# Kernel tuning notes

Measured on AMD Instinct MI355X. Metric: run time of the kernel, lower is better.

## Reference

```python
import jax, jax.numpy as jnp
import numpy as np

NR_EMB = 1024
B_COMMITMENT = 1.0


def setup_inputs() -> dict:
    key = jax.random.key(0)
    k1, k2 = jax.random.split(key)
    inpt = jax.random.normal(k1, (64, 2048, 64), dtype=jnp.float32)
    # VarianceScaling(uniform) over shape (D, K): limit = sqrt(3*scale/fan_in), scale=1, fan_in=D
    D = 64
    limit = np.sqrt(3.0 / D).astype(np.float32)
    emb_mtrx = jax.random.uniform(k2, (D, NR_EMB), dtype=jnp.float32, minval=-limit, maxval=limit)
    return {"inpt": inpt, "emb_mtrx": emb_mtrx}


def reference(inpt, emb_mtrx):
    D = inpt.shape[-1]
    x = inpt.reshape(-1, D)  # [N, D]
    dist = (jnp.sum(x * x, axis=1, keepdims=True)
            - 2.0 * (x @ emb_mtrx)
            + jnp.sum(emb_mtrx * emb_mtrx, axis=0, keepdims=True))
    idx = jnp.argmax(-dist, axis=1)  # [N]
    # avg_probs = mean of one-hot over N == normalized histogram (same math, no N x K one-hot)
    avg_probs = jnp.bincount(idx, length=NR_EMB).astype(inpt.dtype) / x.shape[0]
    perplexity = jnp.exp(-jnp.sum(avg_probs * jnp.log(avg_probs + 1e-10)))
    idx_nd = idx.reshape(inpt.shape[:-1])  # [B, T]
    q = jnp.take(emb_mtrx.T, idx_nd, axis=0)  # gather codebook rows -> [B, T, D]
    l_commitment = jnp.mean((jax.lax.stop_gradient(q) - inpt) ** 2)
    l_codebook = jnp.mean((q - jax.lax.stop_gradient(inpt)) ** 2)
    loss = B_COMMITMENT * l_commitment + l_codebook
    q = inpt + jax.lax.stop_gradient(q - inpt)  # straight-through estimator
    return q, loss, perplexity
```

## Files before the change

kernel.cpp:

```cpp
#include <hip/hip_runtime.h>

#define NROWS 131072
#define D 64
#define K 1024

typedef __attribute__((ext_vector_type(8))) short short8;
typedef __attribute__((ext_vector_type(4))) float f32x4;
typedef unsigned int u32;


__device__ __forceinline__ unsigned short f2bf_rne(float f) {
    u32 u = __float_as_uint(f);
    u += 0x7fff + ((u >> 16) & 1);
    return (unsigned short)(u >> 16);
}

__device__ __forceinline__ float b2f(short s) {
    return __uint_as_float(((u32)(unsigned short)s) << 16);
}

__global__ __launch_bounds__(256) void prep_kernel(const float* __restrict__ E,
                                                   unsigned short* __restrict__ ehT,
                                                   float* __restrict__ e2g,
                                                   int* __restrict__ hist) {
    __shared__ float ps[4][64];
    const int lane = threadIdx.x & 63;
    const int w = threadIdx.x >> 6;
    const int k = blockIdx.x * 64 + lane;
    float s = 0.f;
#pragma unroll
    for (int half = 0; half < 2; ++half) {
        short8 h8;
#pragma unroll
        for (int j = 0; j < 8; ++j) {
            float v = E[(w * 16 + half * 8 + j) * K + k];
            s = fmaf(v, v, s);
            h8[j] = (short)f2bf_rne(v);
        }
        *(short8*)(ehT + (size_t)k * D + w * 16 + half * 8) = h8;
    }
    ps[w][lane] = s;
    __syncthreads();
    if (w == 0) e2g[k] = -0.5f * (ps[0][lane] + ps[1][lane] + ps[2][lane] + ps[3][lane]);
    if (threadIdx.x < 64) hist[blockIdx.x * 64 + threadIdx.x] = 0;
}

__global__ __launch_bounds__(1024) void score_kernel(const float* __restrict__ X,
                                                     const unsigned short* __restrict__ ehT,
                                                     const float* __restrict__ e2g,
                                                     int* __restrict__ hist,
                                                     float* __restrict__ wavesum,
                                                     float* __restrict__ q) {
    __shared__ unsigned short xbuf[2][8192];
    __shared__ float mrg[2][128 * 17];
    __shared__ int idxl[2][128];
    __shared__ float redL[16];

    const int tid = threadIdx.x;
    const int wave = tid >> 6;
    const int lane = tid & 63;
    const int quad = lane >> 4;
    const int lc = lane & 15;
    const size_t row0 = (size_t)blockIdx.x * 512;

    const int st = tid >> 7, so = (tid >> 4) & 7, sl = tid & 15;
    const int rowl = st * 16 + sl;
    const float* sbase = X + (row0 + (size_t)rowl) * D + so * 8;

    {
        float4 La = *(const float4*)(sbase);
        float4 Lb = *(const float4*)(sbase + 4);
        union { u32 u[4]; short8 v; } pk;
        pk.u[0] = __builtin_amdgcn_perm(__float_as_uint(La.y), __float_as_uint(La.x), 0x07060302);
        pk.u[1] = __builtin_amdgcn_perm(__float_as_uint(La.w), __float_as_uint(La.z), 0x07060302);
        pk.u[2] = __builtin_amdgcn_perm(__float_as_uint(Lb.y), __float_as_uint(Lb.x), 0x07060302);
        pk.u[3] = __builtin_amdgcn_perm(__float_as_uint(Lb.w), __float_as_uint(Lb.z), 0x07060302);
        *(short8*)((char*)&xbuf[0][0] + tid * 16) = pk.v;
    }

    const int cbase = wave * 64;
    short8 ae[4][2];
    f32x4 e2f[4];
#pragma unroll
    for (int ct = 0; ct < 4; ++ct) {
        const unsigned short* ap = ehT + ((size_t)(cbase + ct * 16 + lc) << 6) + quad * 8;
        ae[ct][0] = *(const short8*)(ap);
        ae[ct][1] = *(const short8*)(ap + 32);
        e2f[ct] = *(const f32x4*)(e2g + cbase + ct * 16 + quad * 4);
    }
    const u32 cb0 = (u32)(cbase + quad * 4);

    __syncthreads();

    float ls = 0.f;
    for (int c = 0; c < 4; ++c) {
        const int cur = c & 1;
        float4 La, Lb;
        if (c < 3) {
            La = *(const float4*)(sbase + (c + 1) * 8192);
            Lb = *(const float4*)(sbase + (c + 1) * 8192 + 4);
        }

        float bt8[8];
        const char* bb = (const char*)&xbuf[cur][0];
#pragma unroll 2
        for (int t = 0; t < 8; ++t) {
            const char* bp = bb + t * 2048 + quad * 256 + lc * 16;
            short8 b0 = *(const short8*)(bp);
            short8 b1 = *(const short8*)(bp + 1024);
            float bt = -3.4e38f;
#pragma unroll
            for (int ct = 0; ct < 4; ++ct) {
                f32x4 acc = __builtin_amdgcn_mfma_f32_16x16x32_bf16(ae[ct][0], b0, e2f[ct], 0, 0, 0);
                acc = __builtin_amdgcn_mfma_f32_16x16x32_bf16(ae[ct][1], b1, acc, 0, 0, 0);
                float p0 = __uint_as_float((__float_as_uint(acc[0]) & 0xFFFFFC00u) | (cb0 + ct * 16 + 0));
                float p1 = __uint_as_float((__float_as_uint(acc[1]) & 0xFFFFFC00u) | (cb0 + ct * 16 + 1));
                float p2 = __uint_as_float((__float_as_uint(acc[2]) & 0xFFFFFC00u) | (cb0 + ct * 16 + 2));
                float p3 = __uint_as_float((__float_as_uint(acc[3]) & 0xFFFFFC00u) | (cb0 + ct * 16 + 3));
                bt = fmaxf(bt, fmaxf(p0, p1));
                bt = fmaxf(bt, fmaxf(p2, p3));
            }
            bt8[t] = bt;
        }
#pragma unroll
        for (int t = 0; t < 8; ++t) {
            float bt = bt8[t];
            bt = fmaxf(bt, __shfl_xor(bt, 16, 64));
            bt = fmaxf(bt, __shfl_xor(bt, 32, 64));
            if (lane < 16) mrg[cur][(t * 16 + lane) * 17 + wave] = bt;
        }
        __syncthreads();

        if (tid < 128) {
            float m = mrg[cur][tid * 17];
#pragma unroll
            for (int w = 1; w < 16; ++w) m = fmaxf(m, mrg[cur][tid * 17 + w]);
            int kk = (int)(__float_as_uint(m) & 1023u);
            idxl[cur][tid] = kk;
            atomicAdd(&hist[kk], 1);
        }
        if (c < 3) {
            union { u32 u[4]; short8 v; } pk;
            pk.u[0] = __builtin_amdgcn_perm(__float_as_uint(La.y), __float_as_uint(La.x), 0x07060302);
            pk.u[1] = __builtin_amdgcn_perm(__float_as_uint(La.w), __float_as_uint(La.z), 0x07060302);
            pk.u[2] = __builtin_amdgcn_perm(__float_as_uint(Lb.y), __float_as_uint(Lb.x), 0x07060302);
            pk.u[3] = __builtin_amdgcn_perm(__float_as_uint(Lb.w), __float_as_uint(Lb.z), 0x07060302);
            *(short8*)((char*)&xbuf[cur ^ 1][0] + tid * 16) = pk.v;
        }
        __syncthreads();

        {
            int kk = idxl[cur][rowl];
            short8 ev = *(const short8*)(ehT + ((size_t)kk << 6) + so * 8);
            short8 xv = *(const short8*)(&xbuf[cur][tid * 8]);
            float4 qa, qb;
            float e0, dd;
            e0 = b2f(ev[0]); dd = e0 - b2f(xv[0]); ls = fmaf(dd, dd, ls); qa.x = e0;
            e0 = b2f(ev[1]); dd = e0 - b2f(xv[1]); ls = fmaf(dd, dd, ls); qa.y = e0;
            e0 = b2f(ev[2]); dd = e0 - b2f(xv[2]); ls = fmaf(dd, dd, ls); qa.z = e0;
            e0 = b2f(ev[3]); dd = e0 - b2f(xv[3]); ls = fmaf(dd, dd, ls); qa.w = e0;
            e0 = b2f(ev[4]); dd = e0 - b2f(xv[4]); ls = fmaf(dd, dd, ls); qb.x = e0;
            e0 = b2f(ev[5]); dd = e0 - b2f(xv[5]); ls = fmaf(dd, dd, ls); qb.y = e0;
            e0 = b2f(ev[6]); dd = e0 - b2f(xv[6]); ls = fmaf(dd, dd, ls); qb.z = e0;
            e0 = b2f(ev[7]); dd = e0 - b2f(xv[7]); ls = fmaf(dd, dd, ls); qb.w = e0;
            float* qp = q + (row0 + (size_t)(c * 128 + rowl)) * D + so * 8;
            *(float4*)(qp) = qa;
            *(float4*)(qp + 4) = qb;
        }
    }

    for (int off = 32; off > 0; off >>= 1) ls += __shfl_down(ls, off, 64);
    if (lane == 0) redL[wave] = ls;
    __syncthreads();
    if (tid == 0) {
        float L = 0.f;
#pragma unroll
        for (int i = 0; i < 16; ++i) L += redL[i];
        wavesum[blockIdx.x] = L;
    }
}

__global__ __launch_bounds__(1024) void finalize_kernel(const int* __restrict__ hist,
                                                        const float* __restrict__ wavesum,
                                                        float* __restrict__ out) {
    __shared__ float redH[16], redL[16];
    int tid = threadIdx.x;
    float p = (float)hist[tid] * (1.0f / (float)NROWS);
    float term = p * logf(p + 1e-10f);
    float ls = (tid < 256) ? wavesum[tid] : 0.f;
    for (int off = 32; off > 0; off >>= 1) {
        term += __shfl_down(term, off, 64);
        ls += __shfl_down(ls, off, 64);
    }
    int lane = tid & 63, wid = tid >> 6;
    if (lane == 0) { redH[wid] = term; redL[wid] = ls; }
    __syncthreads();
    if (tid == 0) {
        float H = 0.f, L = 0.f;
#pragma unroll
        for (int i = 0; i < 16; ++i) { H += redH[i]; L += redL[i]; }
        out[(size_t)NROWS * D + 0] = 2.0f * (L / (float)(NROWS * D));
        out[(size_t)NROWS * D + 1] = expf(-H);
    }
}

extern "C" void kernel_launch(void* const* d_in, const int* in_sizes, int n_in,
                              void* d_out, int out_size, void* d_ws, size_t ws_size,
                              hipStream_t stream) {
    const float* X = (const float*)d_in[0];
    const float* E = (const float*)d_in[1];
    float* out = (float*)d_out;

    char* w = (char*)d_ws;
    unsigned short* ehT = (unsigned short*)(w + 0);
    float* e2g          = (float*)(w + 131072);
    int* hist           = (int*)(w + 135168);
    float* wavesum      = (float*)(w + 139264);

    prep_kernel<<<16, 256, 0, stream>>>(E, ehT, e2g, hist);
    score_kernel<<<NROWS / 512, 1024, 0, stream>>>(X, ehT, e2g, hist, wavesum, out);
    finalize_kernel<<<1, 1024, 0, stream>>>(hist, wavesum, out);
}
```

Measured before the change: 123.9 us.

## Process rows in two 256-row superchunks to halve block barriers

The score loop now handles two 128-row chunks per iteration (256 rows), so there are two super-iterations instead of four. This halves the number of __syncthreads and merge phases. X staging is quadruple-buffered: two chunks are preloaded up front and the other two are loaded during the first super-iteration. The shuffle-reduce of the per-tile max is moved into the MFMA loop, and the histogram atomics are moved after the barrier. In exchange, LDS use grows (64KB of xbuf plus a larger mrg), which can lower occupancy, and the prefetch is less deeply overlapped since chunks 2 and 3 are both loaded at the start.

```diff
diff --git a/kernel.cpp b/kernel.cpp
--- a/kernel.cpp
+++ b/kernel.cpp
@@ -51,9 +51,9 @@
                                                      int* __restrict__ hist,
                                                      float* __restrict__ wavesum,
                                                      float* __restrict__ q) {
-    __shared__ unsigned short xbuf[2][8192];
-    __shared__ float mrg[2][128 * 17];
-    __shared__ int idxl[2][128];
+    __shared__ unsigned short xbuf[4][8192];
+    __shared__ float mrg[256 * 17];
+    __shared__ int idxl[2][256];
     __shared__ float redL[16];
 
     const int tid = threadIdx.x;
@@ -68,14 +68,21 @@
     const float* sbase = X + (row0 + (size_t)rowl) * D + so * 8;
 
     {
-        float4 La = *(const float4*)(sbase);
-        float4 Lb = *(const float4*)(sbase + 4);
+        float4 L0a = *(const float4*)(sbase);
+        float4 L0b = *(const float4*)(sbase + 4);
+        float4 L1a = *(const float4*)(sbase + 8192);
+        float4 L1b = *(const float4*)(sbase + 8192 + 4);
         union { u32 u[4]; short8 v; } pk;
-        pk.u[0] = __builtin_amdgcn_perm(__float_as_uint(La.y), __float_as_uint(La.x), 0x07060302);
-        pk.u[1] = __builtin_amdgcn_perm(__float_as_uint(La.w), __float_as_uint(La.z), 0x07060302);
-        pk.u[2] = __builtin_amdgcn_perm(__float_as_uint(Lb.y), __float_as_uint(Lb.x), 0x07060302);
-        pk.u[3] = __builtin_amdgcn_perm(__float_as_uint(Lb.w), __float_as_uint(Lb.z), 0x07060302);
+        pk.u[0] = __builtin_amdgcn_perm(__float_as_uint(L0a.y), __float_as_uint(L0a.x), 0x07060302);
+        pk.u[1] = __builtin_amdgcn_perm(__float_as_uint(L0a.w), __float_as_uint(L0a.z), 0x07060302);
+        pk.u[2] = __builtin_amdgcn_perm(__float_as_uint(L0b.y), __float_as_uint(L0b.x), 0x07060302);
+        pk.u[3] = __builtin_amdgcn_perm(__float_as_uint(L0b.w), __float_as_uint(L0b.z), 0x07060302);
         *(short8*)((char*)&xbuf[0][0] + tid * 16) = pk.v;
+        pk.u[0] = __builtin_amdgcn_perm(__float_as_uint(L1a.y), __float_as_uint(L1a.x), 0x07060302);
+        pk.u[1] = __builtin_amdgcn_perm(__float_as_uint(L1a.w), __float_as_uint(L1a.z), 0x07060302);
+        pk.u[2] = __builtin_amdgcn_perm(__float_as_uint(L1b.y), __float_as_uint(L1b.x), 0x07060302);
+        pk.u[3] = __builtin_amdgcn_perm(__float_as_uint(L1b.w), __float_as_uint(L1b.z), 0x07060302);
+        *(short8*)((char*)&xbuf[1][0] + tid * 16) = pk.v;
     }
 
     const int cbase = wave * 64;
@@ -93,18 +100,18 @@
     __syncthreads();
 
     float ls = 0.f;
-    for (int c = 0; c < 4; ++c) {
-        const int cur = c & 1;
-        float4 La, Lb;
-        if (c < 3) {
-            La = *(const float4*)(sbase + (c + 1) * 8192);
-            Lb = *(const float4*)(sbase + (c + 1) * 8192 + 4);
-        }
-
-        float bt8[8];
-        const char* bb = (const char*)&xbuf[cur][0];
+    float4 P2a, P2b, P3a, P3b;
+    for (int sc = 0; sc < 2; ++sc) {
+        if (sc == 0) {
+            P2a = *(const float4*)(sbase + 2 * 8192);
+            P2b = *(const float4*)(sbase + 2 * 8192 + 4);
+            P3a = *(const float4*)(sbase + 3 * 8192);
+            P3b = *(const float4*)(sbase + 3 * 8192 + 4);
+        }
+
+        const char* bb = (const char*)&xbuf[sc * 2][0];
 #pragma unroll 2
-        for (int t = 0; t < 8; ++t) {
+        for (int t = 0; t < 16; ++t) {
             const char* bp = bb + t * 2048 + quad * 256 + lc * 16;
             short8 b0 = *(const short8*)(bp);
             short8 b1 = *(const short8*)(bp + 1024);
@@ -120,39 +127,41 @@
                 bt = fmaxf(bt, fmaxf(p0, p1));
                 bt = fmaxf(bt, fmaxf(p2, p3));
             }
-            bt8[t] = bt;
-        }
-#pragma unroll
-        for (int t = 0; t < 8; ++t) {
-            float bt = bt8[t];
             bt = fmaxf(bt, __shfl_xor(bt, 16, 64));
             bt = fmaxf(bt, __shfl_xor(bt, 32, 64));
-            if (lane < 16) mrg[cur][(t * 16 + lane) * 17 + wave] = bt;
+            if (lane < 16) mrg[(t * 16 + lane) * 17 + wave] = bt;
         }
         __syncthreads();
 
-        if (tid < 128) {
-            float m = mrg[cur][tid * 17];
-#pragma unroll
-            for (int w = 1; w < 16; ++w) m = fmaxf(m, mrg[cur][tid * 17 + w]);
-            int kk = (int)(__float_as_uint(m) & 1023u);
-            idxl[cur][tid] = kk;
-            atomicAdd(&hist[kk], 1);
-        }
-        if (c < 3) {
+        if (tid < 256) {
+            float m = mrg[tid * 17];
+#pragma unroll
+            for (int w = 1; w < 16; ++w) m = fmaxf(m, mrg[tid * 17 + w]);
+            idxl[sc][tid] = (int)(__float_as_uint(m) & 1023u);
+        }
+        if (sc == 0) {
             union { u32 u[4]; short8 v; } pk;
-            pk.u[0] = __builtin_amdgcn_perm(__float_as_uint(La.y), __float_as_uint(La.x), 0x07060302);
-            pk.u[1] = __builtin_amdgcn_perm(__float_as_uint(La.w), __float_as_uint(La.z), 0x07060302);
-            pk.u[2] = __builtin_amdgcn_perm(__float_as_uint(Lb.y), __float_as_uint(Lb.x), 0x07060302);
-            pk.u[3] = __builtin_amdgcn_perm(__float_as_uint(Lb.w), __float_as_uint(Lb.z), 0x07060302);
-            *(short8*)((char*)&xbuf[cur ^ 1][0] + tid * 16) = pk.v;
+            pk.u[0] = __builtin_amdgcn_perm(__float_as_uint(P2a.y), __float_as_uint(P2a.x), 0x07060302);
+            pk.u[1] = __builtin_amdgcn_perm(__float_as_uint(P2a.w), __float_as_uint(P2a.z), 0x07060302);
+            pk.u[2] = __builtin_amdgcn_perm(__float_as_uint(P2b.y), __float_as_uint(P2b.x), 0x07060302);
+            pk.u[3] = __builtin_amdgcn_perm(__float_as_uint(P2b.w), __float_as_uint(P2b.z), 0x07060302);
+            *(short8*)((char*)&xbuf[2][0] + tid * 16) = pk.v;
+            pk.u[0] = __builtin_amdgcn_perm(__float_as_uint(P3a.y), __float_as_uint(P3a.x), 0x07060302);
+            pk.u[1] = __builtin_amdgcn_perm(__float_as_uint(P3a.w), __float_as_uint(P3a.z), 0x07060302);
+            pk.u[2] = __builtin_amdgcn_perm(__float_as_uint(P3b.y), __float_as_uint(P3b.x), 0x07060302);
+            pk.u[3] = __builtin_amdgcn_perm(__float_as_uint(P3b.w), __float_as_uint(P3b.z), 0x07060302);
+            *(short8*)((char*)&xbuf[3][0] + tid * 16) = pk.v;
         }
         __syncthreads();
 
-        {
-            int kk = idxl[cur][rowl];
+        if (tid < 256) atomicAdd(&hist[idxl[sc][tid]], 1);
+
+#pragma unroll
+        for (int h = 0; h < 2; ++h) {
+            const int cc = sc * 2 + h;
+            int kk = idxl[sc][h * 128 + rowl];
             short8 ev = *(const short8*)(ehT + ((size_t)kk << 6) + so * 8);
-            short8 xv = *(const short8*)(&xbuf[cur][tid * 8]);
+            short8 xv = *(const short8*)(&xbuf[cc][tid * 8]);
             float4 qa, qb;
             float e0, dd;
             e0 = b2f(ev[0]); dd = e0 - b2f(xv[0]); ls = fmaf(dd, dd, ls); qa.x = e0;
@@ -163,7 +172,7 @@
             e0 = b2f(ev[5]); dd = e0 - b2f(xv[5]); ls = fmaf(dd, dd, ls); qb.y = e0;
             e0 = b2f(ev[6]); dd = e0 - b2f(xv[6]); ls = fmaf(dd, dd, ls); qb.z = e0;
             e0 = b2f(ev[7]); dd = e0 - b2f(xv[7]); ls = fmaf(dd, dd, ls); qb.w = e0;
-            float* qp = q + (row0 + (size_t)(c * 128 + rowl)) * D + so * 8;
+            float* qp = q + (row0 + (size_t)(cc * 128 + rowl)) * D + so * 8;
             *(float4*)(qp) = qa;
             *(float4*)(qp + 4) = qb;
         }
```

After: 127.5 us. 1.03x slower.

## Fuse codebook prep into score kernel and use per-block shared histograms

Applied to the files above, without the earlier changes.

Removes the separate prep kernel: each score block now reads the fp32 codebook directly, converts it to bf16 in registers and computes the codebook norms with wave shuffles. Global histogram atomics are replaced by shared-memory atomics, with each block writing its own histogram, which the finalize kernel sums across 256 blocks. The gather for q reads fp32 codebook columns with a strided access pattern instead of the packed bf16 rows. This saves one launch and the global atomic contention, but adds redundant codebook conversion in every block, uncoalesced strided gathers, and a 1 MB per-block histogram reduction done by a single finalize block.

```diff
diff --git a/kernel.cpp b/kernel.cpp
--- a/kernel.cpp
+++ b/kernel.cpp
@@ -3,6 +3,7 @@
 #define NROWS 131072
 #define D 64
 #define K 1024
+#define NBLK 256
 
 typedef __attribute__((ext_vector_type(8))) short short8;
 typedef __attribute__((ext_vector_type(4))) float f32x4;
@@ -19,41 +20,15 @@
     return __uint_as_float(((u32)(unsigned short)s) << 16);
 }
 
-__global__ __launch_bounds__(256) void prep_kernel(const float* __restrict__ E,
-                                                   unsigned short* __restrict__ ehT,
-                                                   float* __restrict__ e2g,
-                                                   int* __restrict__ hist) {
-    __shared__ float ps[4][64];
-    const int lane = threadIdx.x & 63;
-    const int w = threadIdx.x >> 6;
-    const int k = blockIdx.x * 64 + lane;
-    float s = 0.f;
-#pragma unroll
-    for (int half = 0; half < 2; ++half) {
-        short8 h8;
-#pragma unroll
-        for (int j = 0; j < 8; ++j) {
-            float v = E[(w * 16 + half * 8 + j) * K + k];
-            s = fmaf(v, v, s);
-            h8[j] = (short)f2bf_rne(v);
-        }
-        *(short8*)(ehT + (size_t)k * D + w * 16 + half * 8) = h8;
-    }
-    ps[w][lane] = s;
-    __syncthreads();
-    if (w == 0) e2g[k] = -0.5f * (ps[0][lane] + ps[1][lane] + ps[2][lane] + ps[3][lane]);
-    if (threadIdx.x < 64) hist[blockIdx.x * 64 + threadIdx.x] = 0;
-}
-
 __global__ __launch_bounds__(1024) void score_kernel(const float* __restrict__ X,
-                                                     const unsigned short* __restrict__ ehT,
-                                                     const float* __restrict__ e2g,
-                                                     int* __restrict__ hist,
+                                                     const float* __restrict__ E,
+                                                     int* __restrict__ bhist,
                                                      float* __restrict__ wavesum,
                                                      float* __restrict__ q) {
     __shared__ unsigned short xbuf[2][8192];
     __shared__ float mrg[2][128 * 17];
     __shared__ int idxl[2][128];
+    __shared__ int lhist[1024];
     __shared__ float redL[16];
 
     const int tid = threadIdx.x;
@@ -62,6 +37,8 @@
     const int quad = lane >> 4;
     const int lc = lane & 15;
     const size_t row0 = (size_t)blockIdx.x * 512;
+
+    lhist[tid] = 0;
 
     const int st = tid >> 7, so = (tid >> 4) & 7, sl = tid & 15;
     const int rowl = st * 16 + sl;
@@ -81,12 +58,34 @@
     const int cbase = wave * 64;
     short8 ae[4][2];
     f32x4 e2f[4];
-#pragma unroll
-    for (int ct = 0; ct < 4; ++ct) {
-        const unsigned short* ap = ehT + ((size_t)(cbase + ct * 16 + lc) << 6) + quad * 8;
-        ae[ct][0] = *(const short8*)(ap);
-        ae[ct][1] = *(const short8*)(ap + 32);
-        e2f[ct] = *(const f32x4*)(e2g + cbase + ct * 16 + quad * 4);
+    {
+        float tot[4];
+#pragma unroll
+        for (int ct = 0; ct < 4; ++ct) {
+            const int code = cbase + ct * 16 + lc;
+            float p = 0.f;
+#pragma unroll
+            for (int ks = 0; ks < 2; ++ks) {
+                union { u32 u[4]; short8 v; } pk;
+#pragma unroll
+                for (int jj = 0; jj < 4; ++jj) {
+                    float va = E[(size_t)(ks * 32 + quad * 8 + 2 * jj) * K + code];
+                    float vb = E[(size_t)(ks * 32 + quad * 8 + 2 * jj + 1) * K + code];
+                    p = fmaf(va, va, p);
+                    p = fmaf(vb, vb, p);
+                    pk.u[jj] = ((u32)f2bf_rne(vb) << 16) | (u32)f2bf_rne(va);
+                }
+                ae[ct][ks] = pk.v;
+            }
+            p += __shfl_xor(p, 16, 64);
+            p += __shfl_xor(p, 32, 64);
+            tot[ct] = p;
+        }
+#pragma unroll
+        for (int ct = 0; ct < 4; ++ct)
+#pragma unroll
+            for (int r = 0; r < 4; ++r)
+                e2f[ct][r] = -0.5f * __shfl(tot[ct], quad * 4 + r, 64);
     }
     const u32 cb0 = (u32)(cbase + quad * 4);
 
@@ -137,7 +136,7 @@
             for (int w = 1; w < 16; ++w) m = fmaxf(m, mrg[cur][tid * 17 + w]);
             int kk = (int)(__float_as_uint(m) & 1023u);
             idxl[cur][tid] = kk;
-            atomicAdd(&hist[kk], 1);
+            atomicAdd(&lhist[kk], 1);
         }
         if (c < 3) {
             union { u32 u[4]; short8 v; } pk;
@@ -151,23 +150,30 @@
 
         {
             int kk = idxl[cur][rowl];
-            short8 ev = *(const short8*)(ehT + ((size_t)kk << 6) + so * 8);
             short8 xv = *(const short8*)(&xbuf[cur][tid * 8]);
             float4 qa, qb;
             float e0, dd;
-            e0 = b2f(ev[0]); dd = e0 - b2f(xv[0]); ls = fmaf(dd, dd, ls); qa.x = e0;
-            e0 = b2f(ev[1]); dd = e0 - b2f(xv[1]); ls = fmaf(dd, dd, ls); qa.y = e0;
-            e0 = b2f(ev[2]); dd = e0 - b2f(xv[2]); ls = fmaf(dd, dd, ls); qa.z = e0;
-            e0 = b2f(ev[3]); dd = e0 - b2f(xv[3]); ls = fmaf(dd, dd, ls); qa.w = e0;
-            e0 = b2f(ev[4]); dd = e0 - b2f(xv[4]); ls = fmaf(dd, dd, ls); qb.x = e0;
-            e0 = b2f(ev[5]); dd = e0 - b2f(xv[5]); ls = fmaf(dd, dd, ls); qb.y = e0;
-            e0 = b2f(ev[6]); dd = e0 - b2f(xv[6]); ls = fmaf(dd, dd, ls); qb.z = e0;
-            e0 = b2f(ev[7]); dd = e0 - b2f(xv[7]); ls = fmaf(dd, dd, ls); qb.w = e0;
+#pragma unroll
+            for (int i = 0; i < 4; ++i) {
+                e0 = b2f((short)f2bf_rne(E[(size_t)(so * 8 + i) * K + kk]));
+                dd = e0 - b2f(xv[i]);
+                ls = fmaf(dd, dd, ls);
+                ((float*)&qa)[i] = e0;
+            }
+#pragma unroll
+            for (int i = 0; i < 4; ++i) {
+                e0 = b2f((short)f2bf_rne(E[(size_t)(so * 8 + 4 + i) * K + kk]));
+                dd = e0 - b2f(xv[4 + i]);
+                ls = fmaf(dd, dd, ls);
+                ((float*)&qb)[i] = e0;
+            }
             float* qp = q + (row0 + (size_t)(c * 128 + rowl)) * D + so * 8;
             *(float4*)(qp) = qa;
             *(float4*)(qp + 4) = qb;
         }
     }
+
+    bhist[blockIdx.x * 1024 + tid] = lhist[tid];
 
     for (int off = 32; off > 0; off >>= 1) ls += __shfl_down(ls, off, 64);
     if (lane == 0) redL[wave] = ls;
@@ -180,14 +186,17 @@
     }
 }
 
-__global__ __launch_bounds__(1024) void finalize_kernel(const int* __restrict__ hist,
+__global__ __launch_bounds__(1024) void finalize_kernel(const int* __restrict__ bhist,
                                                         const float* __restrict__ wavesum,
                                                         float* __restrict__ out) {
     __shared__ float redH[16], redL[16];
     int tid = threadIdx.x;
-    float p = (float)hist[tid] * (1.0f / (float)NROWS);
+    int h = 0;
+#pragma unroll 4
+    for (int b = 0; b < NBLK; ++b) h += bhist[b * 1024 + tid];
+    float p = (float)h * (1.0f / (float)NROWS);
     float term = p * logf(p + 1e-10f);
-    float ls = (tid < 256) ? wavesum[tid] : 0.f;
+    float ls = (tid < NBLK) ? wavesum[tid] : 0.f;
     for (int off = 32; off > 0; off >>= 1) {
         term += __shfl_down(term, off, 64);
         ls += __shfl_down(ls, off, 64);
@@ -212,12 +221,9 @@
     float* out = (float*)d_out;
 
     char* w = (char*)d_ws;
-    unsigned short* ehT = (unsigned short*)(w + 0);
-    float* e2g          = (float*)(w + 131072);
-    int* hist           = (int*)(w + 135168);
-    float* wavesum      = (float*)(w + 139264);
-
-    prep_kernel<<<16, 256, 0, stream>>>(E, ehT, e2g, hist);
-    score_kernel<<<NROWS / 512, 1024, 0, stream>>>(X, ehT, e2g, hist, wavesum, out);
-    finalize_kernel<<<1, 1024, 0, stream>>>(hist, wavesum, out);
-}
+    int* bhist    = (int*)(w + 0);
+    float* wavesum = (float*)(w + 1048576);
+
+    score_kernel<<<NBLK, 1024, 0, stream>>>(X, E, bhist, wavesum, out);
+    finalize_kernel<<<1, 1024, 0, stream>>>(bhist, wavesum, out);
+}
```

Measured after the change: 142.9 us. 15.4% more time.
